# Kernel optimization log

Measured on AMD Instinct MI355X. Metric: run time of the kernel, lower is better.

## Reference

```python
import jax, jax.numpy as jnp
import numpy as np

N_QUBITS = 4
N_LAYERS = 3
N_OUTPUTS = 4
BATCH = 1048576


def _ry(t):
    # RY(t) = [[cos(t/2), -sin(t/2)], [sin(t/2), cos(t/2)]]; t may be scalar or (B,)
    c = jnp.cos(t / 2)
    s = jnp.sin(t / 2)
    m = jnp.stack([jnp.stack([c, -s], -1), jnp.stack([s, c], -1)], -2)
    return m.astype(jnp.complex64)


def _rx(t):
    c = jnp.cos(t / 2).astype(jnp.complex64)
    s = jnp.sin(t / 2).astype(jnp.complex64)
    return jnp.stack([jnp.stack([c, -1j * s], -1), jnp.stack([-1j * s, c], -1)], -2)


def _rz(t):
    e = jnp.exp(-1j * t.astype(jnp.complex64) / 2)  # exp(-i t/2)
    z = jnp.zeros_like(e)
    return jnp.stack([jnp.stack([e, z], -1), jnp.stack([z, jnp.conj(e)], -1)], -2)


def _apply_1q(state, U, q):
    # shared 2x2 gate U on wire q; state: (B, 2,2,2,2)
    s = jnp.moveaxis(state, q + 1, -1)
    s = jnp.einsum('ij,...j->...i', U, s)
    return jnp.moveaxis(s, -1, q + 1)


def _apply_1q_batched(state, U, q):
    # per-sample 2x2 gate U: (B,2,2) on wire q
    s = jnp.moveaxis(state, q + 1, -1)  # (B, ..., 2)
    s = jnp.einsum('bij,b...j->b...i', U, s)
    return jnp.moveaxis(s, -1, q + 1)


def _apply_cnot(state, c, t):
    s = jnp.moveaxis(state, (c + 1, t + 1), (-2, -1))  # (..., ctrl, tgt)
    s = jnp.stack([s[..., 0, :], s[..., 1, ::-1]], axis=-2)
    return jnp.moveaxis(s, (-2, -1), (c + 1, t + 1))


def setup_inputs() -> dict:
    key = jax.random.key(0)
    kx, kw = jax.random.split(key)
    x = jax.random.normal(kx, (BATCH, 2), dtype=jnp.float32)
    weights = jax.random.normal(kw, (N_LAYERS, N_QUBITS, 3), dtype=jnp.float32) * 0.1
    return {"x": x, "weights": weights}


def reference(x, weights):
    B = x.shape[0]
    # |0...0> state, batched
    state = jnp.zeros((B,) + (2,) * N_QUBITS, jnp.complex64)
    state = state.at[(slice(None),) + (0,) * N_QUBITS].set(1.0)
    # data encoding: RY(inputs[i % 2]) on wire i (per-sample angles)
    for i in range(N_QUBITS):
        state = _apply_1q_batched(state, _ry(x[:, i % 2]), i)
    # variational layers (shared angles)
    for l in range(N_LAYERS):
        for i in range(N_QUBITS):
            state = _apply_1q(state, _rx(weights[l, i, 0]), i)
            state = _apply_1q(state, _ry(weights[l, i, 1]), i)
            state = _apply_1q(state, _rz(weights[l, i, 2]), i)
        for i in range(N_QUBITS):
            state = _apply_cnot(state, i, (i + 1) % N_QUBITS)
    probs = state.real ** 2 + state.imag ** 2  # (B,2,2,2,2)
    outs = []
    for q in range(N_OUTPUTS):
        p = jnp.moveaxis(probs, q + 1, 1).reshape(B, 2, -1).sum(-1)
        outs.append(p[:, 0] - p[:, 1])  # <Z_q>
    return jnp.stack(outs, -1)  # (B, N_OUTPUTS)
```

## Files before the change

kernel.cpp:

```cpp
#include <hip/hip_runtime.h>
#include <hip/hip_bf16.h>


__global__ __launch_bounds__(256) void qnn_setup(const float* __restrict__ w,
                                                 float* __restrict__ C_out) {
    __shared__ float Ur[16][16];
    __shared__ float Ui[16][16];
    __shared__ float Csh[100];
    const int t = threadIdx.x;

    if (t < 100) Csh[t] = 0.0f;

    if (t < 16) {
        float ar[16], ai[16];
#pragma unroll
        for (int i = 0; i < 16; i++) { ar[i] = (i == t) ? 1.0f : 0.0f; ai[i] = 0.0f; }

#pragma unroll
        for (int l = 0; l < 3; l++) {
#pragma unroll
            for (int wq = 0; wq < 4; wq++) {
                const int st = 1 << (3 - wq);
                float th, s, c;
                th = w[(l * 4 + wq) * 3 + 0] * 0.5f;
                __sincosf(th, &s, &c);
#pragma unroll
                for (int lo = 0; lo < 16; lo++) if (!(lo & st)) {
                    const int hi = lo | st;
                    const float arl = ar[lo], ail = ai[lo], arh = ar[hi], aih = ai[hi];
                    ar[lo] = c * arl + s * aih;
                    ai[lo] = c * ail - s * arh;
                    ar[hi] = c * arh + s * ail;
                    ai[hi] = c * aih - s * arl;
                }
                th = w[(l * 4 + wq) * 3 + 1] * 0.5f;
                __sincosf(th, &s, &c);
#pragma unroll
                for (int lo = 0; lo < 16; lo++) if (!(lo & st)) {
                    const int hi = lo | st;
                    const float arl = ar[lo], ail = ai[lo], arh = ar[hi], aih = ai[hi];
                    ar[lo] = c * arl - s * arh;
                    ai[lo] = c * ail - s * aih;
                    ar[hi] = s * arl + c * arh;
                    ai[hi] = s * ail + c * aih;
                }
                th = w[(l * 4 + wq) * 3 + 2] * 0.5f;
                __sincosf(th, &s, &c);
#pragma unroll
                for (int lo = 0; lo < 16; lo++) if (!(lo & st)) {
                    const int hi = lo | st;
                    const float arl = ar[lo], ail = ai[lo], arh = ar[hi], aih = ai[hi];
                    ar[lo] = c * arl + s * ail;
                    ai[lo] = c * ail - s * arl;
                    ar[hi] = c * arh - s * aih;
                    ai[hi] = c * aih + s * arh;
                }
            }
#pragma unroll
            for (int ci = 0; ci < 4; ci++) {
                const int cst = 1 << (3 - ci);
                const int tst = 1 << (3 - ((ci + 1) & 3));
#pragma unroll
                for (int k = 0; k < 16; k++) if ((k & cst) && !(k & tst)) {
                    const int k2 = k | tst;
                    const float tr = ar[k], ti = ai[k];
                    ar[k] = ar[k2]; ai[k] = ai[k2];
                    ar[k2] = tr;    ai[k2] = ti;
                }
            }
        }
#pragma unroll
        for (int i = 0; i < 16; i++) { Ur[i][t] = ar[i]; Ui[i][t] = ai[i]; }
    }
    __syncthreads();

    {
        const int i = t >> 4;
        const int j = t & 15;
        float m0 = 0.f, m1 = 0.f, m2 = 0.f, m3 = 0.f;
#pragma unroll
        for (int k = 0; k < 16; k++) {
            const float r = Ur[k][i] * Ur[k][j] + Ui[k][i] * Ui[k][j];
            m0 += ((k >> 3) & 1) ? -r : r;
            m1 += ((k >> 2) & 1) ? -r : r;
            m2 += ((k >> 1) & 1) ? -r : r;
            m3 += ((k >> 0) & 1) ? -r : r;
        }
        const int mm = ((i >> 3) & 1) + ((i >> 1) & 1) + ((j >> 3) & 1) + ((j >> 1) & 1);
        const int nn = ((i >> 2) & 1) + (i & 1) + ((j >> 2) & 1) + (j & 1);
        atomicAdd(&Csh[0 * 25 + mm * 5 + nn], m0);
        atomicAdd(&Csh[1 * 25 + mm * 5 + nn], m1);
        atomicAdd(&Csh[2 * 25 + mm * 5 + nn], m2);
        atomicAdd(&Csh[3 * 25 + mm * 5 + nn], m3);
    }
    __syncthreads();
    if (t < 100) C_out[t] = Csh[t];
}


__device__ __forceinline__ float2 mul2(float2 a, float2 b) {
    return make_float2(a.x * b.x, a.y * b.y);
}
__device__ __forceinline__ float2 fma2(float s, float2 a, float2 b) {
    return make_float2(fmaf(s, a.x, b.x), fmaf(s, a.y, b.y));
}
__device__ __forceinline__ float2 fma22(float2 s, float2 a, float2 b) {
    return make_float2(fmaf(s.x, a.x, b.x), fmaf(s.y, a.y, b.y));
}

constexpr int PAIRS = 2;

__global__ __launch_bounds__(256) void qnn_batch(const float4* __restrict__ x,
                                                 const float* __restrict__ C,
                                                 float4* __restrict__ out,
                                                 int npairs, int B) {
    float cf[100];
#pragma unroll
    for (int i = 0; i < 100; i++) cf[i] = C[i];

    const int base = blockIdx.x * (256 * PAIRS) + threadIdx.x;
#pragma unroll
    for (int k = 0; k < PAIRS; k++) {
        const int p = base + k * 256;
        if (p < npairs) {
            const float4 xv = x[p];
            float2 s0, c0, s1, c1;
            __sincosf(xv.x * 0.5f, &s0.x, &c0.x);
            __sincosf(xv.z * 0.5f, &s0.y, &c0.y);
            __sincosf(xv.y * 0.5f, &s1.x, &c1.x);
            __sincosf(xv.w * 0.5f, &s1.y, &c1.y);

            const float2 cc0 = mul2(c0, c0), ss0 = mul2(s0, s0), cs0 = mul2(c0, s0);
            const float2 cc1 = mul2(c1, c1), ss1 = mul2(s1, s1), cs1 = mul2(c1, s1);
            float2 p0[5] = { mul2(cc0, cc0), mul2(cc0, cs0), mul2(cs0, cs0),
                             mul2(cs0, ss0), mul2(ss0, ss0) };
            float2 p1[5] = { mul2(cc1, cc1), mul2(cc1, cs1), mul2(cs1, cs1),
                             mul2(cs1, ss1), mul2(ss1, ss1) };
            float2 o[4];
#pragma unroll
            for (int q = 0; q < 4; q++) {
                float2 acc = make_float2(0.0f, 0.0f);
#pragma unroll
                for (int m = 0; m < 5; m++) {
                    float2 inner = make_float2(0.0f, 0.0f);
#pragma unroll
                    for (int n = 0; n < 5; n++)
                        inner = fma2(cf[q * 25 + m * 5 + n], p1[n], inner);
                    acc = fma22(p0[m], inner, acc);
                }
                o[q] = acc;
            }
            out[2 * p]     = make_float4(o[0].x, o[1].x, o[2].x, o[3].x);
            out[2 * p + 1] = make_float4(o[0].y, o[1].y, o[2].y, o[3].y);
        }
    }

    if ((B & 1) && blockIdx.x == 0 && threadIdx.x == 0) {
        const int b = B - 1;
        const float2 xt = ((const float2*)x)[b];
        float st0, ct0, st1, ct1;
        __sincosf(xt.x * 0.5f, &st0, &ct0);
        __sincosf(xt.y * 0.5f, &st1, &ct1);
        const float cc0 = ct0 * ct0, ss0 = st0 * st0, cs0 = ct0 * st0;
        const float cc1 = ct1 * ct1, ss1 = st1 * st1, cs1 = ct1 * st1;
        float q0[5] = { cc0 * cc0, cc0 * cs0, cs0 * cs0, cs0 * ss0, ss0 * ss0 };
        float q1[5] = { cc1 * cc1, cc1 * cs1, cs1 * cs1, cs1 * ss1, ss1 * ss1 };
        float o[4];
#pragma unroll
        for (int q = 0; q < 4; q++) {
            float acc = 0.0f;
#pragma unroll
            for (int m = 0; m < 5; m++) {
                float inner = 0.0f;
#pragma unroll
                for (int n = 0; n < 5; n++)
                    inner = fmaf(cf[q * 25 + m * 5 + n], q1[n], inner);
                acc = fmaf(q0[m], inner, acc);
            }
            o[q] = acc;
        }
        out[b] = make_float4(o[0], o[1], o[2], o[3]);
    }
}

extern "C" void kernel_launch(void* const* d_in, const int* in_sizes, int n_in,
                              void* d_out, int out_size, void* d_ws, size_t ws_size,
                              hipStream_t stream) {
    const float* x = (const float*)d_in[0];
    const float* w = (const float*)d_in[1];
    float* C = (float*)d_ws;
    const int B = in_sizes[0] / 2;

    qnn_setup<<<1, 256, 0, stream>>>(w, C);

    const int npairs = B >> 1;
    int grid = (npairs + 256 * PAIRS - 1) / (256 * PAIRS);
    if (grid < 1) grid = 1;
    qnn_batch<<<grid, 256, 0, stream>>>((const float4*)x, C, (float4*)d_out,
                                        npairs, B);
}
```

Baseline: 74.28 us.

## Fuse coefficient setup into batch kernel, recomputing per block

Merges the single-block setup kernel into the batch kernel, so each block recomputes the 16x16 circuit unitary and the 100 coefficients in shared memory before processing 1024 samples. This removes one kernel launch and the global-memory round trip for the coefficients. In exchange every one of 1024 blocks repeats the small unitary simulation and a shared-memory reduction with atomics. The sample mapping also changes to strided float2 loads per thread, replacing the earlier float4 pair loads.

```diff
diff --git a/kernel.cpp b/kernel.cpp
--- a/kernel.cpp
+++ b/kernel.cpp
@@ -2,11 +2,23 @@
 #include <hip/hip_bf16.h>
 
 
-__global__ __launch_bounds__(256) void qnn_setup(const float* __restrict__ w,
-                                                 float* __restrict__ C_out) {
+__device__ __forceinline__ float2 mul2(float2 a, float2 b) {
+    return make_float2(a.x * b.x, a.y * b.y);
+}
+__device__ __forceinline__ float2 fma2(float s, float2 a, float2 b) {
+    return make_float2(fmaf(s, a.x, b.x), fmaf(s, a.y, b.y));
+}
+__device__ __forceinline__ float2 fma22(float2 s, float2 a, float2 b) {
+    return make_float2(fmaf(s.x, a.x, b.x), fmaf(s.y, a.y, b.y));
+}
+
+__global__ __launch_bounds__(256) void qnn_fused(const float2* __restrict__ x,
+                                                 const float* __restrict__ w,
+                                                 float4* __restrict__ out,
+                                                 int B) {
     __shared__ float Ur[16][16];
     __shared__ float Ui[16][16];
-    __shared__ float Csh[100];
+    __shared__ __align__(16) float Csh[100];
     const int t = threadIdx.x;
 
     if (t < 100) Csh[t] = 0.0f;
@@ -94,41 +106,31 @@
         atomicAdd(&Csh[3 * 25 + mm * 5 + nn], m3);
     }
     __syncthreads();
-    if (t < 100) C_out[t] = Csh[t];
-}
-
-
-__device__ __forceinline__ float2 mul2(float2 a, float2 b) {
-    return make_float2(a.x * b.x, a.y * b.y);
-}
-__device__ __forceinline__ float2 fma2(float s, float2 a, float2 b) {
-    return make_float2(fmaf(s, a.x, b.x), fmaf(s, a.y, b.y));
-}
-__device__ __forceinline__ float2 fma22(float2 s, float2 a, float2 b) {
-    return make_float2(fmaf(s.x, a.x, b.x), fmaf(s.y, a.y, b.y));
-}
-
-constexpr int PAIRS = 2;
-
-__global__ __launch_bounds__(256) void qnn_batch(const float4* __restrict__ x,
-                                                 const float* __restrict__ C,
-                                                 float4* __restrict__ out,
-                                                 int npairs, int B) {
+
     float cf[100];
 #pragma unroll
-    for (int i = 0; i < 100; i++) cf[i] = C[i];
-
-    const int base = blockIdx.x * (256 * PAIRS) + threadIdx.x;
-#pragma unroll
-    for (int k = 0; k < PAIRS; k++) {
-        const int p = base + k * 256;
-        if (p < npairs) {
-            const float4 xv = x[p];
+    for (int i = 0; i < 25; i++) {
+        const float4 v = ((const float4*)Csh)[i];
+        cf[4 * i + 0] = v.x;
+        cf[4 * i + 1] = v.y;
+        cf[4 * i + 2] = v.z;
+        cf[4 * i + 3] = v.w;
+    }
+
+    const int bs = blockIdx.x * 1024;
+
+    if (bs + 1024 <= B) {
+#pragma unroll
+        for (int k = 0; k < 2; k++) {
+            const int sA = bs + k * 512 + t;
+            const int sB = sA + 256;
+            const float2 xA = x[sA];
+            const float2 xB = x[sB];
             float2 s0, c0, s1, c1;
-            __sincosf(xv.x * 0.5f, &s0.x, &c0.x);
-            __sincosf(xv.z * 0.5f, &s0.y, &c0.y);
-            __sincosf(xv.y * 0.5f, &s1.x, &c1.x);
-            __sincosf(xv.w * 0.5f, &s1.y, &c1.y);
+            __sincosf(xA.x * 0.5f, &s0.x, &c0.x);
+            __sincosf(xB.x * 0.5f, &s0.y, &c0.y);
+            __sincosf(xA.y * 0.5f, &s1.x, &c1.x);
+            __sincosf(xB.y * 0.5f, &s1.y, &c1.y);
 
             const float2 cc0 = mul2(c0, c0), ss0 = mul2(s0, s0), cs0 = mul2(c0, s0);
             const float2 cc1 = mul2(c1, c1), ss1 = mul2(s1, s1), cs1 = mul2(c1, s1);
@@ -150,36 +152,39 @@
                 }
                 o[q] = acc;
             }
-            out[2 * p]     = make_float4(o[0].x, o[1].x, o[2].x, o[3].x);
-            out[2 * p + 1] = make_float4(o[0].y, o[1].y, o[2].y, o[3].y);
-        }
-    }
-
-    if ((B & 1) && blockIdx.x == 0 && threadIdx.x == 0) {
-        const int b = B - 1;
-        const float2 xt = ((const float2*)x)[b];
-        float st0, ct0, st1, ct1;
-        __sincosf(xt.x * 0.5f, &st0, &ct0);
-        __sincosf(xt.y * 0.5f, &st1, &ct1);
-        const float cc0 = ct0 * ct0, ss0 = st0 * st0, cs0 = ct0 * st0;
-        const float cc1 = ct1 * ct1, ss1 = st1 * st1, cs1 = ct1 * st1;
-        float q0[5] = { cc0 * cc0, cc0 * cs0, cs0 * cs0, cs0 * ss0, ss0 * ss0 };
-        float q1[5] = { cc1 * cc1, cc1 * cs1, cs1 * cs1, cs1 * ss1, ss1 * ss1 };
-        float o[4];
-#pragma unroll
-        for (int q = 0; q < 4; q++) {
-            float acc = 0.0f;
-#pragma unroll
-            for (int m = 0; m < 5; m++) {
-                float inner = 0.0f;
-#pragma unroll
-                for (int n = 0; n < 5; n++)
-                    inner = fmaf(cf[q * 25 + m * 5 + n], q1[n], inner);
-                acc = fmaf(q0[m], inner, acc);
-            }
-            o[q] = acc;
-        }
-        out[b] = make_float4(o[0], o[1], o[2], o[3]);
+            out[sA] = make_float4(o[0].x, o[1].x, o[2].x, o[3].x);
+            out[sB] = make_float4(o[0].y, o[1].y, o[2].y, o[3].y);
+        }
+    } else {
+#pragma unroll
+        for (int k = 0; k < 4; k++) {
+            const int s = bs + k * 256 + t;
+            if (s < B) {
+                const float2 xv = x[s];
+                float st0, ct0, st1, ct1;
+                __sincosf(xv.x * 0.5f, &st0, &ct0);
+                __sincosf(xv.y * 0.5f, &st1, &ct1);
+                const float cc0 = ct0 * ct0, ss0 = st0 * st0, cs0 = ct0 * st0;
+                const float cc1 = ct1 * ct1, ss1 = st1 * st1, cs1 = ct1 * st1;
+                float q0[5] = { cc0 * cc0, cc0 * cs0, cs0 * cs0, cs0 * ss0, ss0 * ss0 };
+                float q1[5] = { cc1 * cc1, cc1 * cs1, cs1 * cs1, cs1 * ss1, ss1 * ss1 };
+                float o[4];
+#pragma unroll
+                for (int q = 0; q < 4; q++) {
+                    float acc = 0.0f;
+#pragma unroll
+                    for (int m = 0; m < 5; m++) {
+                        float inner = 0.0f;
+#pragma unroll
+                        for (int n = 0; n < 5; n++)
+                            inner = fmaf(cf[q * 25 + m * 5 + n], q1[n], inner);
+                        acc = fmaf(q0[m], inner, acc);
+                    }
+                    o[q] = acc;
+                }
+                out[s] = make_float4(o[0], o[1], o[2], o[3]);
+            }
+        }
     }
 }
 
@@ -188,14 +193,9 @@
                               hipStream_t stream) {
     const float* x = (const float*)d_in[0];
     const float* w = (const float*)d_in[1];
-    float* C = (float*)d_ws;
     const int B = in_sizes[0] / 2;
 
-    qnn_setup<<<1, 256, 0, stream>>>(w, C);
-
-    const int npairs = B >> 1;
-    int grid = (npairs + 256 * PAIRS - 1) / (256 * PAIRS);
+    int grid = (B + 1023) / 1024;
     if (grid < 1) grid = 1;
-    qnn_batch<<<grid, 256, 0, stream>>>((const float4*)x, C, (float4*)d_out,
-                                        npairs, B);
-}
+    qnn_fused<<<grid, 256, 0, stream>>>((const float2*)x, w, (float4*)d_out, B);
+}
```

After: 84.13 us. 1.13x slower.
